# Optimization experiments

Hardware: AMD Instinct MI355X
Metric: run time of the kernel (lower is better)

## Reference

```python
import jax, jax.numpy as jnp
import numpy as np

S, B, E, H, V, L = 512, 64, 512, 768, 32000, 32
PAD_WORD, PAD_LABEL = 1, 0
PAD_BIAS = 10000.0


def _linear_init(key, fin, fout):
    # matches torch nn.Linear default U(-1/sqrt(fin), 1/sqrt(fin))
    kw, kb = jax.random.split(key)
    s = 1.0 / np.sqrt(fin)
    W = jax.random.uniform(kw, (fin, fout), minval=-s, maxval=s, dtype=jnp.float32)
    b = jax.random.uniform(kb, (fout,), minval=-s, maxval=s, dtype=jnp.float32)
    return W, b


def setup_inputs() -> dict:
    key = jax.random.key(0)
    ks = jax.random.split(key, 9)
    tokens = jax.random.randint(ks[0], (S, B), 0, V, dtype=jnp.int32)
    tags = jax.random.randint(ks[1], (S, B), 0, L, dtype=jnp.int32)
    embedding = jax.random.normal(ks[2], (V, E), dtype=jnp.float32)
    # gate order along the 4H axis: r, f, g, o (matches the 8 separate Linears, stacked)
    Wi_f, bi_f = _linear_init(ks[3], E, 4 * H)
    Wh_f, bh_f = _linear_init(ks[4], H, 4 * H)
    Wi_b, bi_b = _linear_init(ks[5], E, 4 * H)
    Wh_b, bh_b = _linear_init(ks[6], H, 4 * H)
    Wout, bout = _linear_init(ks[7], 2 * H, L)
    return {"tokens": tokens, "tags": tags, "embedding": embedding,
            "Wi_f": Wi_f, "bi_f": bi_f, "Wh_f": Wh_f, "bh_f": bh_f,
            "Wi_b": Wi_b, "bi_b": bi_b, "Wh_b": Wh_b, "bh_b": bh_b,
            "Wout": Wout, "bout": bout}


def _forward(tokens, embedding, Wi_f, bi_f, Wh_f, bh_f, Wi_b, bi_b, Wh_b, bh_b, Wout, bout):
    emb = embedding[tokens]                      # [S,B,E]
    b = tokens.shape[1]
    h = emb.shape[-1] * 0 + Wh_f.shape[0]
    # ---- forward direction: true LSTM-style recurrence ----
    xf = jnp.einsum('sbe,eg->sbg', emb, Wi_f) + bi_f   # [S,B,4H] precomputed input gates

    def step_f(carry, x):
        hid, c = carry
        g = x + hid @ Wh_f + bh_f
        r, f, gg, o = jnp.split(g, 4, axis=-1)
        c = jax.nn.sigmoid(f) * c + jax.nn.sigmoid(r) * jnp.tanh(gg)
        hid = jax.nn.sigmoid(o) * jnp.tanh(c)
        return (hid, c), hid

    z = jnp.zeros((b, h), dtype=emb.dtype)
    (hT, _), hs_f = jax.lax.scan(step_f, (z, z), xf)   # hs_f: [S,B,H]

    # ---- backward direction: source never updates `hidden`, so the hidden
    # projection uses the CONSTANT final forward hidden hT at every step.
    gb = jnp.einsum('sbe,eg->sbg', emb, Wi_b) + bi_b + hT @ Wh_b + bh_b  # [S,B,4H]
    r2, f2, g2, o2 = jnp.split(gb, 4, axis=-1)
    r2 = jax.nn.sigmoid(r2); f2 = jax.nn.sigmoid(f2)
    g2 = jnp.tanh(g2);       o2 = jax.nn.sigmoid(o2)

    def step_b(c2, gates):
        r, f, g, o = gates
        c2 = f * c2 + r * g
        return c2, o * jnp.tanh(c2)

    _, hs_b = jax.lax.scan(step_b, z, (r2, f2, g2, o2), reverse=True)  # [S,B,H], original order

    outputs = jnp.concatenate([hs_f, hs_b], axis=-1)   # [S,B,2H]
    out = outputs @ Wout + bout                        # [S,B,L]
    pad_mask = (tokens == PAD_WORD).astype(out.dtype)
    out = out.at[:, :, PAD_LABEL].add(pad_mask * PAD_BIAS)
    return out


def reference(tokens, tags, embedding, Wi_f, bi_f, Wh_f, bh_f, Wi_b, bi_b, Wh_b, bh_b, Wout, bout):
    del tags  # unused in forward, kept for signature fidelity
    return _forward(tokens, embedding, Wi_f, bi_f, Wh_f, bh_f, Wi_b, bi_b, Wh_b, bh_b, Wout, bout)
```

## Files before the change

### kernel.cpp

```cpp
#include <hip/hip_runtime.h>
#include <hip/hip_bf16.h>
#include <stdint.h>

typedef __attribute__((ext_vector_type(8))) short bf16x8;
typedef __attribute__((ext_vector_type(4))) float f32x4;
typedef __attribute__((ext_vector_type(4))) unsigned int u32x4;
typedef unsigned long long ull_t;

#define S_LEN 512
#define B_DIM 64
#define E_DIM 512
#define H_DIM 768
#define G4    3072
#define H2    1536
#define M_ROWS 32768
#define CHUNK 128
#define CM    8192
#define SLW   24
#define WPS   8
#define WPR   256
#define RWRD  4096
#define PSTR  16384
#define KRES  640
#define KREG  4
#define WROW  648
#define NTILES 1536
#define EROW  520

__device__ __forceinline__ float sigmf_(float x) { return 1.0f / (1.0f + __expf(-x)); }
__device__ __forceinline__ float tanhf2(float x) {
  x = fminf(fmaxf(x, -20.0f), 20.0f);
  float e = __expf(2.0f * x);
  return (e - 1.0f) / (e + 1.0f);
}
__device__ __forceinline__ float bfu(unsigned short u) { return __uint_as_float((unsigned)u << 16); }
__device__ __forceinline__ unsigned short packbf(float a) {
  __hip_bfloat16 t = __float2bfloat16(a);
  unsigned short b;
  __builtin_memcpy(&b, &t, 2);
  return b;
}

__global__ __launch_bounds__(256) void k_gather(const int* __restrict__ tokens,
                                                const float* __restrict__ emb,
                                                __hip_bfloat16* __restrict__ out) {
  const int t = blockIdx.x * 256 + threadIdx.x;
  const int e0 = t * 8;
  const int row = e0 >> 9;
  const int k = e0 & 511;
  const int tok = tokens[row];
  const float4* p = (const float4*)(emb + (size_t)tok * E_DIM + k);
  const float4 v0 = p[0], v1 = p[1];
  __align__(16) __hip_bfloat16 tmp[8];
  tmp[0] = __float2bfloat16(v0.x); tmp[1] = __float2bfloat16(v0.y);
  tmp[2] = __float2bfloat16(v0.z); tmp[3] = __float2bfloat16(v0.w);
  tmp[4] = __float2bfloat16(v1.x); tmp[5] = __float2bfloat16(v1.y);
  tmp[6] = __float2bfloat16(v1.z); tmp[7] = __float2bfloat16(v1.w);
  *(bf16x8*)(out + (size_t)t * 8) = *(const bf16x8*)tmp;
}

__global__ __launch_bounds__(256) void k_transpose_cast(const float* __restrict__ src,
                                                        __hip_bfloat16* __restrict__ dst,
                                                        int Rs, int Cs) {
  __shared__ float tile[32][33];
  const int tx = threadIdx.x & 31, ty = threadIdx.x >> 5;
  const int c0 = blockIdx.x * 32, r0 = blockIdx.y * 32;
  #pragma unroll
  for (int i = ty; i < 32; i += 8)
    tile[i][tx] = src[(size_t)(r0 + i) * Cs + c0 + tx];
  __syncthreads();
  #pragma unroll
  for (int i = ty; i < 32; i += 8)
    dst[(size_t)(c0 + i) * Rs + r0 + tx] = __float2bfloat16(tile[tx][i]);
}

__global__ __launch_bounds__(256) void k_bias(const float* __restrict__ bi,
                                              const float* __restrict__ bh,
                                              float* __restrict__ bias) {
  const int n = blockIdx.x * 256 + threadIdx.x;
  bias[n] = bi[n] + bh[n];
}

__device__ __forceinline__ void gemm_tile_e(char* pool, int tile,
                                            const __hip_bfloat16* __restrict__ A,
                                            const __hip_bfloat16* __restrict__ BT,
                                            const float* __restrict__ bias,
                                            __hip_bfloat16* __restrict__ C) {
  auto As = (__hip_bfloat16 (*)[40])pool;
  auto Bs = (__hip_bfloat16 (*)[40])(pool + 10240);
  const int tid = threadIdx.x;
  const int wave = tid >> 6, lane = tid & 63;
  const int q = lane >> 4, lr = lane & 15;
  const int wm = (wave >> 1) * 64, wn = (wave & 1) * 64;
  const int nb = tile % 24, mb = tile / 24;
  const int m0 = mb * 128, n0 = nb * 128;
  const int srow = tid >> 2, skseg = (tid & 3) * 8;

  f32x4 acc[4][4];
  #pragma unroll
  for (int i = 0; i < 4; ++i)
    #pragma unroll
    for (int j = 0; j < 4; ++j) { f32x4 z = {0.f, 0.f, 0.f, 0.f}; acc[i][j] = z; }

  for (int kt = 0; kt < 16; ++kt) {
    __syncthreads();
    const int kbase = kt * 32 + skseg;
    *(bf16x8*)&As[srow][skseg]      = *(const bf16x8*)(A + (size_t)(m0 + srow) * E_DIM + kbase);
    *(bf16x8*)&As[srow + 64][skseg] = *(const bf16x8*)(A + (size_t)(m0 + srow + 64) * E_DIM + kbase);
    *(bf16x8*)&Bs[srow][skseg]      = *(const bf16x8*)(BT + (size_t)(n0 + srow) * E_DIM + kbase);
    *(bf16x8*)&Bs[srow + 64][skseg] = *(const bf16x8*)(BT + (size_t)(n0 + srow + 64) * E_DIM + kbase);
    __syncthreads();
    bf16x8 af[4], bfr[4];
    #pragma unroll
    for (int mt = 0; mt < 4; ++mt) af[mt] = *(const bf16x8*)&As[wm + mt * 16 + lr][q * 8];
    #pragma unroll
    for (int nt = 0; nt < 4; ++nt) bfr[nt] = *(const bf16x8*)&Bs[wn + nt * 16 + lr][q * 8];
    #pragma unroll
    for (int mt = 0; mt < 4; ++mt)
      #pragma unroll
      for (int nt = 0; nt < 4; ++nt)
        acc[mt][nt] = __builtin_amdgcn_mfma_f32_16x16x32_bf16(af[mt], bfr[nt], acc[mt][nt], 0, 0, 0);
  }
  #pragma unroll
  for (int mt = 0; mt < 4; ++mt) {
    #pragma unroll
    for (int nt = 0; nt < 4; ++nt) {
      const int col = n0 + wn + nt * 16 + lr;
      const float bv = bias[col];
      #pragma unroll
      for (int i = 0; i < 4; ++i) {
        const int row = m0 + wm + mt * 16 + q * 4 + i;
        C[(size_t)row * G4 + col] = __float2bfloat16(acc[mt][nt][i] + bv);
      }
    }
  }
}

__device__ __forceinline__ void gemm_tile_g(char* pool, int tile,
                                            const int* __restrict__ tokens_c,
                                            const float* __restrict__ emb,
                                            const __hip_bfloat16* __restrict__ BT,
                                            const float* __restrict__ bias,
                                            __hip_bfloat16* __restrict__ C) {
  auto As = (__hip_bfloat16 (*)[40])pool;
  auto Bs = (__hip_bfloat16 (*)[40])(pool + 10240);
  const int tid = threadIdx.x;
  const int wave = tid >> 6, lane = tid & 63;
  const int q = lane >> 4, lr = lane & 15;
  const int wm = (wave >> 1) * 64, wn = (wave & 1) * 64;
  const int nb = tile % 24, mb = tile / 24;
  const int m0 = mb * 128, n0 = nb * 128;
  const int srow = tid >> 2, skseg = (tid & 3) * 8;
  const int tok0 = tokens_c[m0 + srow];
  const int tok1 = tokens_c[m0 + srow + 64];

  f32x4 acc[4][4];
  #pragma unroll
  for (int i = 0; i < 4; ++i)
    #pragma unroll
    for (int j = 0; j < 4; ++j) { f32x4 z = {0.f, 0.f, 0.f, 0.f}; acc[i][j] = z; }

  for (int kt = 0; kt < 16; ++kt) {
    __syncthreads();
    const int kbase = kt * 32 + skseg;
    {
      const float* ap = emb + (size_t)tok0 * E_DIM + kbase;
      const float4 v0 = *(const float4*)ap, v1 = *(const float4*)(ap + 4);
      __align__(16) __hip_bfloat16 t8[8];
      t8[0] = __float2bfloat16(v0.x); t8[1] = __float2bfloat16(v0.y);
      t8[2] = __float2bfloat16(v0.z); t8[3] = __float2bfloat16(v0.w);
      t8[4] = __float2bfloat16(v1.x); t8[5] = __float2bfloat16(v1.y);
      t8[6] = __float2bfloat16(v1.z); t8[7] = __float2bfloat16(v1.w);
      *(bf16x8*)&As[srow][skseg] = *(const bf16x8*)t8;
    }
    {
      const float* ap = emb + (size_t)tok1 * E_DIM + kbase;
      const float4 v0 = *(const float4*)ap, v1 = *(const float4*)(ap + 4);
      __align__(16) __hip_bfloat16 t8[8];
      t8[0] = __float2bfloat16(v0.x); t8[1] = __float2bfloat16(v0.y);
      t8[2] = __float2bfloat16(v0.z); t8[3] = __float2bfloat16(v0.w);
      t8[4] = __float2bfloat16(v1.x); t8[5] = __float2bfloat16(v1.y);
      t8[6] = __float2bfloat16(v1.z); t8[7] = __float2bfloat16(v1.w);
      *(bf16x8*)&As[srow + 64][skseg] = *(const bf16x8*)t8;
    }
    *(bf16x8*)&Bs[srow][skseg]      = *(const bf16x8*)(BT + (size_t)(n0 + srow) * E_DIM + kbase);
    *(bf16x8*)&Bs[srow + 64][skseg] = *(const bf16x8*)(BT + (size_t)(n0 + srow + 64) * E_DIM + kbase);
    __syncthreads();
    bf16x8 af[4], bfr[4];
    #pragma unroll
    for (int mt = 0; mt < 4; ++mt) af[mt] = *(const bf16x8*)&As[wm + mt * 16 + lr][q * 8];
    #pragma unroll
    for (int nt = 0; nt < 4; ++nt) bfr[nt] = *(const bf16x8*)&Bs[wn + nt * 16 + lr][q * 8];
    #pragma unroll
    for (int mt = 0; mt < 4; ++mt)
      #pragma unroll
      for (int nt = 0; nt < 4; ++nt)
        acc[mt][nt] = __builtin_amdgcn_mfma_f32_16x16x32_bf16(af[mt], bfr[nt], acc[mt][nt], 0, 0, 0);
  }
  #pragma unroll
  for (int mt = 0; mt < 4; ++mt) {
    #pragma unroll
    for (int nt = 0; nt < 4; ++nt) {
      const int col = n0 + wn + nt * 16 + lr;
      const float bv = bias[col];
      #pragma unroll
      for (int i = 0; i < 4; ++i) {
        const int row = m0 + wm + mt * 16 + q * 4 + i;
        C[(size_t)row * G4 + col] = __float2bfloat16(acc[mt][nt][i] + bv);
      }
    }
  }
}

__global__ __launch_bounds__(256) void k_gemm_e(const __hip_bfloat16* __restrict__ A,
                                                const __hip_bfloat16* __restrict__ BT,
                                                const float* __restrict__ bias,
                                                __hip_bfloat16* __restrict__ C) {
  __shared__ __align__(16) char pool[20480];
  gemm_tile_e(pool, blockIdx.x, A, BT, bias, C);
}
__global__ __launch_bounds__(256) void k_gemm_g(const int* __restrict__ tokens_c,
                                                const float* __restrict__ emb,
                                                const __hip_bfloat16* __restrict__ BT,
                                                const float* __restrict__ bias,
                                                __hip_bfloat16* __restrict__ C) {
  __shared__ __align__(16) char pool[20480];
  gemm_tile_g(pool, blockIdx.x, tokens_c, emb, BT, bias, C);
}

__device__ __forceinline__ void out_block8(char* pool, int ob,
                                           const __hip_bfloat16* __restrict__ Hs,
                                           const float* __restrict__ Wout,
                                           const float* __restrict__ bout,
                                           const int* __restrict__ tokens,
                                           float* __restrict__ out) {
  auto rowbuf = (float (*)[1536])pool;
  const int r0 = ob * 8;
  const int tid = threadIdx.x;
  for (int idx = tid; idx < 8 * 1536; idx += 256) {
    const int rr = idx / 1536, k = idx % 1536;
    rowbuf[rr][k] = __bfloat162float(Hs[(size_t)(r0 + rr) * H2 + k]);
  }
  __syncthreads();
  const int l = tid & 31, rr = tid >> 5;
  float acc = bout[l];
  #pragma unroll 8
  for (int k = 0; k < 1536; ++k) acc += rowbuf[rr][k] * Wout[k * 32 + l];
  const int row = r0 + rr;
  if (l == 0 && tokens[row] == 1) acc += 10000.0f;
  out[(size_t)row * 32 + l] = acc;
  __syncthreads();
}

__global__ __launch_bounds__(256) void k_out(const __hip_bfloat16* __restrict__ Hs,
                                             const float* __restrict__ Wout,
                                             const float* __restrict__ bout,
                                             const int* __restrict__ tokens,
                                             float* __restrict__ out) {
  __shared__ __align__(16) char pool[49152];
  out_block8(pool, blockIdx.x, Hs, Wout, bout, tokens, out);
}

__global__ __launch_bounds__(256, 1) void k_fwd_fused(const __hip_bfloat16* __restrict__ X,
                                                      const __hip_bfloat16* __restrict__ WhTf,
                                                      ull_t* __restrict__ hbuf,
                                                      __hip_bfloat16* __restrict__ Hs,
                                                      float* __restrict__ cstate,
                                                      float* __restrict__ hT,
                                                      int chunk,
                                                      const __hip_bfloat16* __restrict__ EmbA,
                                                      const int* __restrict__ tokens_nx,
                                                      const float* __restrict__ emb,
                                                      const __hip_bfloat16* __restrict__ WiT_nx,
                                                      const float* __restrict__ Bias_nx,
                                                      __hip_bfloat16* __restrict__ Xw) {
  __shared__ __align__(16) char pool[155904];
  const int bx = blockIdx.x;

  if (bx >= 128) {
    const int nw = gridDim.x - 128;
    if (EmbA) {
      for (int t = bx - 128; t < NTILES; t += nw)
        gemm_tile_e(pool, t, EmbA, WiT_nx, Bias_nx, Xw);
    } else {
      for (int t = bx - 128; t < NTILES; t += nw)
        gemm_tile_g(pool, t, tokens_nx, emb, WiT_nx, Bias_nx, Xw);
    }
    return;
  }

  unsigned short* wlds = (unsigned short*)pool;
  auto h_stage = (unsigned short (*)[776])(pool + 124416);
  auto g_lds   = (float (*)[16][26])(pool + 149248);

  const int group = bx >> 5;
  const int slice = bx & 31;
  const int r0 = group * 16;
  const int j0 = slice * SLW;
  const int tid = threadIdx.x;
  const int w = tid >> 6;
  const int lane = tid & 63;
  const int q = lane >> 4, lr = lane & 15;
  const int base = chunk * CHUNK;

  const int prow = tid >> 4;
  const int pw   = tid & 15;

  const int row  = tid >> 3;
  const int wloc = tid & 7;
  const int col0 = 3 * wloc;

  for (int c = tid; c < 96 * (KRES / 8); c += 256) {
    const int r = c / (KRES / 8), k8 = c % (KRES / 8);
    const int gate = r / SLW, n = r % SLW;
    const float4 v = *(const float4*)(WhTf + (size_t)(gate * H_DIM + j0 + n) * H_DIM + k8 * 8);
    *(float4*)(wlds + (size_t)r * WROW + k8 * 8) = v;
  }

  const int wn0 = lr;
  const int wn1 = 16 + (lr & 7);
  bf16x8 wr0[KREG], wr1[KREG];
  #pragma unroll
  for (int kk = 0; kk < KREG; ++kk) {
    const int ko = KRES + kk * 32 + q * 8;
    wr0[kk] = *(const bf16x8*)(WhTf + (size_t)(w * H_DIM + j0 + wn0) * H_DIM + ko);
    wr1[kk] = *(const bf16x8*)(WhTf + (size_t)(w * H_DIM + j0 + wn1) * H_DIM + ko);
  }

  float cr[3] = {0.f, 0.f, 0.f};
  if (tid < 128) {
    const float* cs = cstate + (size_t)(r0 + row) * H_DIM + j0 + col0;
    cr[0] = cs[0]; cr[1] = cs[1]; cr[2] = cs[2];
  }

  const unsigned skipbit = ((pw >> 2) == (slice & 3)) ? (1u << (slice >> 2)) : 0u;

  __syncthreads();

  for (int s = 0; s < CHUNK; ++s) {
    const int gs = base + s;

    unsigned short xs[4][3];
    if (tid < 128) {
      const unsigned short* xp = (const unsigned short*)(X + ((size_t)s * B_DIM + r0 + row) * G4 + j0 + col0);
      #pragma unroll
      for (int g = 0; g < 4; ++g)
        #pragma unroll
        for (int j = 0; j < 3; ++j) xs[g][j] = xp[g * H_DIM + j];
    }

    const ull_t* hc = hbuf + ((size_t)(gs & 1)) * PSTR + (size_t)group * RWRD
                    + (size_t)prow * WPR + 2 * pw;
    u32x4 d0 = {0,0,0,0}, d1 = {0,0,0,0}, d2 = {0,0,0,0}, d3 = {0,0,0,0};
    u32x4 d4 = {0,0,0,0}, d5 = {0,0,0,0}, d6 = {0,0,0,0}, d7 = {0,0,0,0};
    const unsigned pollmask = (s == 0) ? 0xFFu : (0xFFu ^ skipbit);
    {
      const unsigned e16 = (unsigned)(unsigned short)gs;
      unsigned need = pollmask;
      long guard = 0;
      for (;;) {
#define POLL_LD(i, dv) \
        if (need & (1u << (i))) \
          asm volatile("global_load_dwordx4 %0, %1, off sc0 sc1" \
                       : "=v"(dv) : "v"(hc + 32 * (i)) : "memory");
        POLL_LD(0, d0) POLL_LD(1, d1) POLL_LD(2, d2) POLL_LD(3, d3)
        POLL_LD(4, d4) POLL_LD(5, d5) POLL_LD(6, d6) POLL_LD(7, d7)
#undef POLL_LD
        asm volatile("s_waitcnt vmcnt(0)"
                     : "+v"(d0), "+v"(d1), "+v"(d2), "+v"(d3),
                       "+v"(d4), "+v"(d5), "+v"(d6), "+v"(d7)
                     :: "memory");
        unsigned nn = 0;
#define POLL_CK(i, dv) \
        if ((need & (1u << (i))) && \
            ((((dv).x & 0xFFFFu) != e16) || (((dv).z & 0xFFFFu) != e16))) nn |= 1u << (i);
        POLL_CK(0, d0) POLL_CK(1, d1) POLL_CK(2, d2) POLL_CK(3, d3)
        POLL_CK(4, d4) POLL_CK(5, d5) POLL_CK(6, d6) POLL_CK(7, d7)
#undef POLL_CK
        need = nn;
        if (!need) break;
        if (++guard > (1L << 20)) break;
        __builtin_amdgcn_s_sleep(1);
      }
    }
    {
#define STAGE_PAIR(i, dv) \
      if (pollmask & (1u << (i))) { \
        unsigned* hp = (unsigned*)&h_stage[prow][6 * pw + 96 * (i)]; \
        hp[0] = ((dv).x >> 16) | ((dv).y << 16); \
        hp[1] = ((dv).y >> 16) | ((dv).z & 0xFFFF0000u); \
        hp[2] = (dv).w; \
      }
      STAGE_PAIR(0, d0) STAGE_PAIR(1, d1) STAGE_PAIR(2, d2) STAGE_PAIR(3, d3)
      STAGE_PAIR(4, d4) STAGE_PAIR(5, d5) STAGE_PAIR(6, d6) STAGE_PAIR(7, d7)
#undef STAGE_PAIR
    }
    __syncthreads();

    f32x4 acc0 = {0.f, 0.f, 0.f, 0.f};
    f32x4 acc1 = {0.f, 0.f, 0.f, 0.f};
    {
      const unsigned short* wb = wlds + (size_t)w * SLW * WROW;
      #pragma unroll
      for (int kt = 0; kt < KRES / 32; ++kt) {
        const int ko = kt * 32 + q * 8;
        const bf16x8 a  = *(const bf16x8*)&h_stage[lr][ko];
        const bf16x8 b0 = *(const bf16x8*)(wb + (size_t)wn0 * WROW + ko);
        const bf16x8 b1 = *(const bf16x8*)(wb + (size_t)wn1 * WROW + ko);
        acc0 = __builtin_amdgcn_mfma_f32_16x16x32_bf16(a, b0, acc0, 0, 0, 0);
        acc1 = __builtin_amdgcn_mfma_f32_16x16x32_bf16(a, b1, acc1, 0, 0, 0);
      }
      #pragma unroll
      for (int kk = 0; kk < KREG; ++kk) {
        const bf16x8 a = *(const bf16x8*)&h_stage[lr][KRES + kk * 32 + q * 8];
        acc0 = __builtin_amdgcn_mfma_f32_16x16x32_bf16(a, wr0[kk], acc0, 0, 0, 0);
        acc1 = __builtin_amdgcn_mfma_f32_16x16x32_bf16(a, wr1[kk], acc1, 0, 0, 0);
      }
    }
    #pragma unroll
    for (int i = 0; i < 4; ++i) g_lds[w][q * 4 + i][lr] = acc0[i];
    if (lr < 8) {
      #pragma unroll
      for (int i = 0; i < 4; ++i) g_lds[w][q * 4 + i][16 + lr] = acc1[i];
    }
    __syncthreads();

    if (tid < 128) {
      float h[3];
      #pragma unroll
      for (int j = 0; j < 3; ++j) {
        const float rv = g_lds[0][row][col0 + j] + bfu(xs[0][j]);
        const float fv = g_lds[1][row][col0 + j] + bfu(xs[1][j]);
        const float gv = g_lds[2][row][col0 + j] + bfu(xs[2][j]);
        const float ov = g_lds[3][row][col0 + j] + bfu(xs[3][j]);
        const float c = sigmf_(fv) * cr[j] + sigmf_(rv) * tanhf2(gv);
        cr[j] = c;
        h[j] = sigmf_(ov) * tanhf2(c);
      }
      const unsigned short b0 = packbf(h[0]), b1 = packbf(h[1]), b2 = packbf(h[2]);
      const ull_t wv = (ull_t)(unsigned short)(gs + 1)
                     | ((ull_t)b0 << 16) | ((ull_t)b1 << 32) | ((ull_t)b2 << 48);
      __hip_atomic_store(hbuf + ((size_t)((gs + 1) & 1)) * PSTR + (size_t)group * RWRD
                         + (size_t)row * WPR + slice * WPS + wloc,
                         wv, __ATOMIC_RELAXED, __HIP_MEMORY_SCOPE_AGENT);
      h_stage[row][j0 + col0]     = b0;
      h_stage[row][j0 + col0 + 1] = b1;
      h_stage[row][j0 + col0 + 2] = b2;
      unsigned short* hsp = (unsigned short*)(Hs + ((size_t)gs * B_DIM + r0 + row) * H2 + j0 + col0);
      hsp[0] = b0; hsp[1] = b1; hsp[2] = b2;
      if (chunk == 3 && s == CHUNK - 1) {
        float* hp = hT + (size_t)(r0 + row) * H_DIM + j0 + col0;
        hp[0] = h[0]; hp[1] = h[1]; hp[2] = h[2];
      }
    }
  }

  if (tid < 128) {
    float* cs = cstate + (size_t)(r0 + row) * H_DIM + j0 + col0;
    cs[0] = cr[0]; cs[1] = cr[1]; cs[2] = cr[2];
  }
}

__global__ __launch_bounds__(256) void k_hTW(const float* __restrict__ hT,
                                             const float* __restrict__ Whb,
                                             float* __restrict__ hTW) {
  const int b = blockIdx.y;
  const int n = blockIdx.x * 256 + threadIdx.x;
  __shared__ float hs[768];
  for (int i = threadIdx.x; i < 768; i += 256) hs[i] = hT[b * 768 + i];
  __syncthreads();
  float acc = 0.f;
  #pragma unroll 4
  for (int k = 0; k < 768; ++k) acc += hs[k] * Whb[(size_t)k * G4 + n];
  hTW[(size_t)b * G4 + n] = acc;
}

__global__ __launch_bounds__(256, 1) void k_bwd_fused3(const __hip_bfloat16* __restrict__ Emb,
                                                       const __hip_bfloat16* __restrict__ WiTb,
                                                       const float* __restrict__ BiasB,
                                                       const float* __restrict__ hTW,
                                                       __hip_bfloat16* __restrict__ Hs,
                                                       float* __restrict__ c2state,
                                                       int chunk) {
  __shared__ __align__(16) unsigned short wlds[96 * EROW];
  __shared__ __align__(16) unsigned short emb_s[2][16][EROW];
  __shared__ float g_lds[4][16][26];

  const int bx = blockIdx.x;
  const int group = bx >> 5;
  const int slice = bx & 31;
  const int r0 = group * 8;
  const int j0 = slice * SLW;
  const int tid = threadIdx.x;
  const int w = tid >> 6;
  const int lane = tid & 63;
  const int q = lane >> 4, lr = lane & 15;
  const int base = chunk * CHUNK;

  for (int c = tid; c < 96 * 64; c += 256) {
    const int r = c >> 6, k8 = c & 63;
    const int gate = r / SLW, n = r % SLW;
    *(float4*)(wlds + (size_t)r * EROW + k8 * 8) =
        *(const float4*)(WiTb + (size_t)(gate * H_DIM + j0 + n) * E_DIM + k8 * 8);
  }

  const int rr = tid >> 3, wloc = tid & 7, col0 = 3 * wloc;
  float hw0[3], hw1[3], hw2[3], hw3[3], c2r[3] = {0.f, 0.f, 0.f};
  if (tid < 64) {
    const int b = r0 + rr;
    #pragma unroll
    for (int j = 0; j < 3; ++j) {
      const int n = j0 + col0 + j;
      hw0[j] = BiasB[n]        + hTW[(size_t)b * G4 + n];
      hw1[j] = BiasB[768 + n]  + hTW[(size_t)b * G4 + 768 + n];
      hw2[j] = BiasB[1536 + n] + hTW[(size_t)b * G4 + 1536 + n];
      hw3[j] = BiasB[2304 + n] + hTW[(size_t)b * G4 + 2304 + n];
      c2r[j] = c2state[(size_t)b * H_DIM + n];
    }
  }
  const int wn0 = lr;
  const int wn1 = 16 + (lr & 7);
  const unsigned short* wb0 = wlds + (size_t)(w * SLW + wn0) * EROW;
  const unsigned short* wb1 = wlds + (size_t)(w * SLW + wn1) * EROW;

  int aa[4], kk8[4];
  #pragma unroll
  for (int i = 0; i < 4; ++i) { aa[i] = (tid + 256 * i) >> 6; kk8[i] = (tid + 256 * i) & 63; }

  bf16x8 pf0, pf1, pf2, pf3;
#define PF_LOAD(t) { \
    pf0 = *(const bf16x8*)(Emb + ((size_t)(base + 2*(t)+1-(aa[0]>>3)) * B_DIM + r0 + (aa[0]&7)) * E_DIM + kk8[0]*8); \
    pf1 = *(const bf16x8*)(Emb + ((size_t)(base + 2*(t)+1-(aa[1]>>3)) * B_DIM + r0 + (aa[1]&7)) * E_DIM + kk8[1]*8); \
    pf2 = *(const bf16x8*)(Emb + ((size_t)(base + 2*(t)+1-(aa[2]>>3)) * B_DIM + r0 + (aa[2]&7)) * E_DIM + kk8[2]*8); \
    pf3 = *(const bf16x8*)(Emb + ((size_t)(base + 2*(t)+1-(aa[3]>>3)) * B_DIM + r0 + (aa[3]&7)) * E_DIM + kk8[3]*8); }

  PF_LOAD(CHUNK / 2 - 1);

  int buf = 0;
  for (int t = CHUNK / 2 - 1; t >= 0; --t) {
    *(bf16x8*)&emb_s[buf][aa[0]][kk8[0] * 8] = pf0;
    *(bf16x8*)&emb_s[buf][aa[1]][kk8[1] * 8] = pf1;
    *(bf16x8*)&emb_s[buf][aa[2]][kk8[2] * 8] = pf2;
    *(bf16x8*)&emb_s[buf][aa[3]][kk8[3] * 8] = pf3;
    if (t > 0) PF_LOAD(t - 1);
    __syncthreads();

    f32x4 a0 = {0.f, 0.f, 0.f, 0.f};
    f32x4 a1 = {0.f, 0.f, 0.f, 0.f};
    #pragma unroll
    for (int kt = 0; kt < 16; ++kt) {
      const int ko = kt * 32 + q * 8;
      const bf16x8 av = *(const bf16x8*)&emb_s[buf][lr][ko];
      const bf16x8 b0 = *(const bf16x8*)(wb0 + ko);
      const bf16x8 b1 = *(const bf16x8*)(wb1 + ko);
      a0 = __builtin_amdgcn_mfma_f32_16x16x32_bf16(av, b0, a0, 0, 0, 0);
      a1 = __builtin_amdgcn_mfma_f32_16x16x32_bf16(av, b1, a1, 0, 0, 0);
    }
    #pragma unroll
    for (int i = 0; i < 4; ++i) g_lds[w][q * 4 + i][lr] = a0[i];
    if (lr < 8) {
      #pragma unroll
      for (int i = 0; i < 4; ++i) g_lds[w][q * 4 + i][16 + lr] = a1[i];
    }
    __syncthreads();

    if (tid < 64) {
      #pragma unroll
      for (int st = 0; st < 2; ++st) {
        const int gs = base + 2 * t + 1 - st;
        const int m = st * 8 + rr;
        unsigned short hb[3];
        #pragma unroll
        for (int j = 0; j < 3; ++j) {
          const float rv = sigmf_(g_lds[0][m][col0 + j] + hw0[j]);
          const float fv = sigmf_(g_lds[1][m][col0 + j] + hw1[j]);
          const float gv = tanhf2(g_lds[2][m][col0 + j] + hw2[j]);
          const float ov = sigmf_(g_lds[3][m][col0 + j] + hw3[j]);
          c2r[j] = fv * c2r[j] + rv * gv;
          hb[j] = packbf(ov * tanhf2(c2r[j]));
        }
        unsigned short* hsp = (unsigned short*)(Hs + ((size_t)gs * B_DIM + r0 + rr) * H2
                                                + H_DIM + j0 + col0);
        hsp[0] = hb[0]; hsp[1] = hb[1]; hsp[2] = hb[2];
      }
    }
    buf ^= 1;
  }
#undef PF_LOAD

  if (tid < 64) {
    #pragma unroll
    for (int j = 0; j < 3; ++j)
      c2state[(size_t)(r0 + rr) * H_DIM + j0 + col0 + j] = c2r[j];
  }
}

__global__ __launch_bounds__(256) void k_bwd_scan(const __hip_bfloat16* __restrict__ X,
                                                  const float* __restrict__ hTW,
                                                  __hip_bfloat16* __restrict__ Hs,
                                                  float* __restrict__ c2state,
                                                  int chunk) {
  const int t = blockIdx.x * 256 + threadIdx.x;
  const int b = t / H_DIM;
  const int j = t % H_DIM;
  const int base = chunk * CHUNK;
  const float hw0 = hTW[(size_t)b * G4 + j];
  const float hw1 = hTW[(size_t)b * G4 + 768 + j];
  const float hw2 = hTW[(size_t)b * G4 + 1536 + j];
  const float hw3 = hTW[(size_t)b * G4 + 2304 + j];
  float c2 = c2state[t];
  for (int s = CHUNK - 1; s >= 0; --s) {
    const size_t xb = ((size_t)s * B_DIM + b) * G4 + j;
    const float r = sigmf_(__bfloat162float(X[xb]) + hw0);
    const float f = sigmf_(__bfloat162float(X[xb + 768]) + hw1);
    const float g = tanhf2(__bfloat162float(X[xb + 1536]) + hw2);
    const float o = sigmf_(__bfloat162float(X[xb + 2304]) + hw3);
    c2 = f * c2 + r * g;
    Hs[((size_t)(base + s) * B_DIM + b) * H2 + H_DIM + j] = __float2bfloat16(o * tanhf2(c2));
  }
  c2state[t] = c2;
}

extern "C" void kernel_launch(void* const* d_in, const int* in_sizes, int n_in,
                              void* d_out, int out_size, void* d_ws, size_t ws_size,
                              hipStream_t stream) {
  const int*   tokens = (const int*)d_in[0];
  const float* emb    = (const float*)d_in[2];
  const float* Wi_f   = (const float*)d_in[3];
  const float* bi_f   = (const float*)d_in[4];
  const float* Wh_f   = (const float*)d_in[5];
  const float* bh_f   = (const float*)d_in[6];
  const float* Wi_b   = (const float*)d_in[7];
  const float* bi_b   = (const float*)d_in[8];
  const float* Wh_b   = (const float*)d_in[9];
  const float* bh_b   = (const float*)d_in[10];
  const float* Wout   = (const float*)d_in[11];
  const float* bout   = (const float*)d_in[12];
  float* out = (float*)d_out;
  char* ws = (char*)d_ws;

  size_t off = 0;
  auto alloc = [&](size_t bytes) { size_t o = off; off += (bytes + 255) & ~(size_t)255; return o; };
  const size_t oHs    = alloc((size_t)M_ROWS * H2 * 2);
  const size_t oX0    = alloc((size_t)CM * G4 * 2);
  const size_t oWhTf  = alloc((size_t)G4 * H_DIM * 2);
  const size_t oWiTf  = alloc((size_t)G4 * E_DIM * 2);
  const size_t oWiTb  = alloc((size_t)G4 * E_DIM * 2);
  const size_t oBiasF = alloc((size_t)G4 * 4);
  const size_t oBiasB = alloc((size_t)G4 * 4);
  const size_t oHbuf  = alloc((size_t)2 * PSTR * 8);
  const size_t oCst   = alloc((size_t)B_DIM * H_DIM * 4);
  const size_t oHT    = alloc((size_t)B_DIM * H_DIM * 4);
  const size_t oHTW   = alloc((size_t)B_DIM * G4 * 4);
  const size_t oC2    = alloc((size_t)B_DIM * H_DIM * 4);
  const size_t oX1    = alloc((size_t)CM * G4 * 2);
  const bool overlap = (off <= ws_size);
  const size_t oEmb   = alloc((size_t)M_ROWS * E_DIM * 2);
  const bool tierA = (off <= ws_size);
  (void)in_sizes; (void)n_in; (void)out_size;

  __hip_bfloat16* Hs   = (__hip_bfloat16*)(ws + oHs);
  __hip_bfloat16* X0   = (__hip_bfloat16*)(ws + oX0);
  __hip_bfloat16* X1   = overlap ? (__hip_bfloat16*)(ws + oX1) : X0;
  __hip_bfloat16* Emb  = tierA ? (__hip_bfloat16*)(ws + oEmb) : (__hip_bfloat16*)nullptr;
  __hip_bfloat16* WhTf = (__hip_bfloat16*)(ws + oWhTf);
  __hip_bfloat16* WiTf = (__hip_bfloat16*)(ws + oWiTf);
  __hip_bfloat16* WiTb = (__hip_bfloat16*)(ws + oWiTb);
  float*          BiasF= (float*)(ws + oBiasF);
  float*          BiasB= (float*)(ws + oBiasB);
  ull_t*          Hbuf = (ull_t*)(ws + oHbuf);
  float*          Cst  = (float*)(ws + oCst);
  float*          HT   = (float*)(ws + oHT);
  float*          HTW  = (float*)(ws + oHTW);
  float*          C2   = (float*)(ws + oC2);

  hipMemsetAsync(ws + oHbuf, 0, (size_t)2 * PSTR * 8, stream);
  hipMemsetAsync(ws + oCst, 0, (size_t)B_DIM * H_DIM * 4, stream);
  hipMemsetAsync(ws + oC2, 0, (size_t)B_DIM * H_DIM * 4, stream);

  if (tierA)
    k_gather<<<8192, 256, 0, stream>>>(tokens, emb, Emb);
  k_transpose_cast<<<dim3(96, 24), 256, 0, stream>>>(Wh_f, WhTf, 768, 3072);
  k_transpose_cast<<<dim3(96, 16), 256, 0, stream>>>(Wi_f, WiTf, 512, 3072);
  k_transpose_cast<<<dim3(96, 16), 256, 0, stream>>>(Wi_b, WiTb, 512, 3072);
  k_bias<<<12, 256, 0, stream>>>(bi_f, bh_f, BiasF);
  k_bias<<<12, 256, 0, stream>>>(bi_b, bh_b, BiasB);

  if (overlap && tierA) {
    k_gemm_e<<<NTILES, 256, 0, stream>>>(Emb, WiTf, BiasF, X0);
    auto EA = [&](int c) { return Emb + (size_t)c * CM * E_DIM; };
    k_fwd_fused<<<240, 256, 0, stream>>>(X0, WhTf, Hbuf, Hs, Cst, HT, 0,
                                         EA(1), tokens, emb, WiTf, BiasF, X1);
    k_fwd_fused<<<240, 256, 0, stream>>>(X1, WhTf, Hbuf, Hs, Cst, HT, 1,
                                         EA(2), tokens, emb, WiTf, BiasF, X0);
    k_fwd_fused<<<240, 256, 0, stream>>>(X0, WhTf, Hbuf, Hs, Cst, HT, 2,
                                         EA(3), tokens, emb, WiTf, BiasF, X1);
    k_fwd_fused<<<128, 256, 0, stream>>>(X1, WhTf, Hbuf, Hs, Cst, HT, 3,
                                         EA(0), tokens, emb, WiTf, BiasF, X0);
    k_hTW<<<dim3(12, 64), 256, 0, stream>>>(HT, Wh_b, HTW);
    k_bwd_fused3<<<256, 256, 0, stream>>>(Emb, WiTb, BiasB, HTW, Hs, C2, 3);
    k_bwd_fused3<<<256, 256, 0, stream>>>(Emb, WiTb, BiasB, HTW, Hs, C2, 2);
    k_bwd_fused3<<<256, 256, 0, stream>>>(Emb, WiTb, BiasB, HTW, Hs, C2, 1);
    k_bwd_fused3<<<256, 256, 0, stream>>>(Emb, WiTb, BiasB, HTW, Hs, C2, 0);
    k_out<<<4096, 256, 0, stream>>>(Hs, Wout, bout, tokens, out);
  } else if (overlap) {
    k_gemm_g<<<NTILES, 256, 0, stream>>>(tokens, emb, WiTf, BiasF, X0);
    k_fwd_fused<<<240, 256, 0, stream>>>(X0, WhTf, Hbuf, Hs, Cst, HT, 0,
                                         nullptr, tokens + 1 * CM, emb, WiTf, BiasF, X1);
    k_fwd_fused<<<240, 256, 0, stream>>>(X1, WhTf, Hbuf, Hs, Cst, HT, 1,
                                         nullptr, tokens + 2 * CM, emb, WiTf, BiasF, X0);
    k_fwd_fused<<<240, 256, 0, stream>>>(X0, WhTf, Hbuf, Hs, Cst, HT, 2,
                                         nullptr, tokens + 3 * CM, emb, WiTf, BiasF, X1);
    k_fwd_fused<<<240, 256, 0, stream>>>(X1, WhTf, Hbuf, Hs, Cst, HT, 3,
                                         nullptr, tokens + 3 * CM, emb, WiTb, BiasB, X0);
    k_hTW<<<dim3(12, 64), 256, 0, stream>>>(HT, Wh_b, HTW);
    k_bwd_scan<<<192, 256, 0, stream>>>(X0, HTW, Hs, C2, 3);
    for (int c = 2; c >= 0; --c) {
      k_gemm_g<<<NTILES, 256, 0, stream>>>(tokens + (size_t)c * CM, emb, WiTb, BiasB, X1);
      k_bwd_scan<<<192, 256, 0, stream>>>(X1, HTW, Hs, C2, c);
    }
    k_out<<<4096, 256, 0, stream>>>(Hs, Wout, bout, tokens, out);
  } else {
    for (int c = 0; c < 4; ++c) {
      k_gemm_g<<<NTILES, 256, 0, stream>>>(tokens + (size_t)c * CM, emb, WiTf, BiasF, X0);
      k_fwd_fused<<<128, 256, 0, stream>>>(X0, WhTf, Hbuf, Hs, Cst, HT, c,
                                           nullptr, tokens, emb, WiTf, BiasF, X0);
    }
    k_hTW<<<dim3(12, 64), 256, 0, stream>>>(HT, Wh_b, HTW);
    for (int c = 3; c >= 0; --c) {
      k_gemm_g<<<NTILES, 256, 0, stream>>>(tokens + (size_t)c * CM, emb, WiTb, BiasB, X0);
      k_bwd_scan<<<192, 256, 0, stream>>>(X0, HTW, Hs, C2, c);
    }
    k_out<<<4096, 256, 0, stream>>>(Hs, Wout, bout, tokens, out);
  }
}
```

Baseline: 3.135 ms.

## Overlap backward input GEMMs and output projection with forward recurrence blocks

When workspace allows two extra gate buffers, the idle GEMM blocks of the forward recurrent kernels also precompute backward-direction input gates for chunks 3 and 2. The first two backward chunks then run as lightweight scans, with extra blocks computing the output projection for the already-finished chunk 3. The final k_out covers only the remaining chunks. The aim is to hide backward GEMM and output-projection work behind the latency-bound forward scan, at the cost of more workspace and more work in the side blocks. It also moves the barrier in bwd_fused3 ahead of the next prefetch.

```diff
diff --git a/kernel.cpp b/kernel.cpp
--- a/kernel.cpp
+++ b/kernel.cpp
@@ -273,7 +273,11 @@
                                                       const float* __restrict__ emb,
                                                       const __hip_bfloat16* __restrict__ WiT_nx,
                                                       const float* __restrict__ Bias_nx,
-                                                      __hip_bfloat16* __restrict__ Xw) {
+                                                      __hip_bfloat16* __restrict__ Xw,
+                                                      const __hip_bfloat16* __restrict__ EmbB,
+                                                      const __hip_bfloat16* __restrict__ WiTb2,
+                                                      const float* __restrict__ BiasB2,
+                                                      __hip_bfloat16* __restrict__ Xb) {
   __shared__ __align__(16) char pool[155904];
   const int bx = blockIdx.x;
 
@@ -285,6 +289,10 @@
     } else {
       for (int t = bx - 128; t < NTILES; t += nw)
         gemm_tile_g(pool, t, tokens_nx, emb, WiT_nx, Bias_nx, Xw);
+    }
+    if (EmbB && Xb) {
+      for (int t = bx - 128; t < NTILES; t += nw)
+        gemm_tile_e(pool, t, EmbB, WiTb2, BiasB2, Xb);
     }
     return;
   }
@@ -542,8 +550,9 @@
     *(bf16x8*)&emb_s[buf][aa[1]][kk8[1] * 8] = pf1;
     *(bf16x8*)&emb_s[buf][aa[2]][kk8[2] * 8] = pf2;
     *(bf16x8*)&emb_s[buf][aa[3]][kk8[3] * 8] = pf3;
+    __syncthreads();
+
     if (t > 0) PF_LOAD(t - 1);
-    __syncthreads();
 
     f32x4 a0 = {0.f, 0.f, 0.f, 0.f};
     f32x4 a1 = {0.f, 0.f, 0.f, 0.f};
@@ -595,12 +604,24 @@
   }
 }
 
-__global__ __launch_bounds__(256) void k_bwd_scan(const __hip_bfloat16* __restrict__ X,
-                                                  const float* __restrict__ hTW,
-                                                  __hip_bfloat16* __restrict__ Hs,
-                                                  float* __restrict__ c2state,
-                                                  int chunk) {
-  const int t = blockIdx.x * 256 + threadIdx.x;
+__global__ __launch_bounds__(256) void k_bwd_scan_o(const __hip_bfloat16* __restrict__ X,
+                                                    const float* __restrict__ hTW,
+                                                    __hip_bfloat16* __restrict__ Hs,
+                                                    float* __restrict__ c2state,
+                                                    int chunk, int out_chunk,
+                                                    const float* __restrict__ Wout,
+                                                    const float* __restrict__ bout,
+                                                    const int* __restrict__ tokens,
+                                                    float* __restrict__ out) {
+  __shared__ __align__(16) char pool[49152];
+  const int bx = blockIdx.x;
+  if (bx >= 192) {
+    if (out_chunk >= 0)
+      for (int ob = bx - 192; ob < 1024; ob += 128)
+        out_block8(pool, out_chunk * 1024 + ob, Hs, Wout, bout, tokens, out);
+    return;
+  }
+  const int t = bx * 256 + threadIdx.x;
   const int b = t / H_DIM;
   const int j = t % H_DIM;
   const int base = chunk * CHUNK;
@@ -657,12 +678,17 @@
   const bool overlap = (off <= ws_size);
   const size_t oEmb   = alloc((size_t)M_ROWS * E_DIM * 2);
   const bool tierA = (off <= ws_size);
+  const size_t oX2    = alloc((size_t)CM * G4 * 2);
+  const size_t oX3    = alloc((size_t)CM * G4 * 2);
+  const bool tierX = (off <= ws_size);
   (void)in_sizes; (void)n_in; (void)out_size;
 
   __hip_bfloat16* Hs   = (__hip_bfloat16*)(ws + oHs);
   __hip_bfloat16* X0   = (__hip_bfloat16*)(ws + oX0);
   __hip_bfloat16* X1   = overlap ? (__hip_bfloat16*)(ws + oX1) : X0;
   __hip_bfloat16* Emb  = tierA ? (__hip_bfloat16*)(ws + oEmb) : (__hip_bfloat16*)nullptr;
+  __hip_bfloat16* X2   = tierX ? (__hip_bfloat16*)(ws + oX2) : (__hip_bfloat16*)nullptr;
+  __hip_bfloat16* X3   = tierX ? (__hip_bfloat16*)(ws + oX3) : (__hip_bfloat16*)nullptr;
   __hip_bfloat16* WhTf = (__hip_bfloat16*)(ws + oWhTf);
   __hip_bfloat16* WiTf = (__hip_bfloat16*)(ws + oWiTf);
   __hip_bfloat16* WiTb = (__hip_bfloat16*)(ws + oWiTb);
@@ -686,17 +712,42 @@
   k_bias<<<12, 256, 0, stream>>>(bi_f, bh_f, BiasF);
   k_bias<<<12, 256, 0, stream>>>(bi_b, bh_b, BiasB);
 
-  if (overlap && tierA) {
+  auto EA = [&](int c) { return Emb + (size_t)c * CM * E_DIM; };
+
+  if (tierX) {
     k_gemm_e<<<NTILES, 256, 0, stream>>>(Emb, WiTf, BiasF, X0);
-    auto EA = [&](int c) { return Emb + (size_t)c * CM * E_DIM; };
     k_fwd_fused<<<240, 256, 0, stream>>>(X0, WhTf, Hbuf, Hs, Cst, HT, 0,
-                                         EA(1), tokens, emb, WiTf, BiasF, X1);
+                                         EA(1), tokens, emb, WiTf, BiasF, X1,
+                                         EA(3), WiTb, BiasB, X2);
     k_fwd_fused<<<240, 256, 0, stream>>>(X1, WhTf, Hbuf, Hs, Cst, HT, 1,
-                                         EA(2), tokens, emb, WiTf, BiasF, X0);
+                                         EA(2), tokens, emb, WiTf, BiasF, X3,
+                                         EA(2), WiTb, BiasB, X0);
+    k_fwd_fused<<<240, 256, 0, stream>>>(X3, WhTf, Hbuf, Hs, Cst, HT, 2,
+                                         EA(3), tokens, emb, WiTf, BiasF, X1,
+                                         nullptr, nullptr, nullptr, nullptr);
+    k_fwd_fused<<<128, 256, 0, stream>>>(X1, WhTf, Hbuf, Hs, Cst, HT, 3,
+                                         EA(0), tokens, emb, WiTf, BiasF, X0,
+                                         nullptr, nullptr, nullptr, nullptr);
+    k_hTW<<<dim3(12, 64), 256, 0, stream>>>(HT, Wh_b, HTW);
+    k_bwd_scan_o<<<320, 256, 0, stream>>>(X2, HTW, Hs, C2, 3, -1, Wout, bout, tokens, out);
+    k_bwd_scan_o<<<320, 256, 0, stream>>>(X0, HTW, Hs, C2, 2, 3, Wout, bout, tokens, out);
+    k_bwd_fused3<<<256, 256, 0, stream>>>(Emb, WiTb, BiasB, HTW, Hs, C2, 1);
+    k_bwd_fused3<<<256, 256, 0, stream>>>(Emb, WiTb, BiasB, HTW, Hs, C2, 0);
+    k_out<<<3072, 256, 0, stream>>>(Hs, Wout, bout, tokens, out);
+  } else if (tierA) {
+    k_gemm_e<<<NTILES, 256, 0, stream>>>(Emb, WiTf, BiasF, X0);
+    k_fwd_fused<<<240, 256, 0, stream>>>(X0, WhTf, Hbuf, Hs, Cst, HT, 0,
+                                         EA(1), tokens, emb, WiTf, BiasF, X1,
+                                         nullptr, nullptr, nullptr, nullptr);
+    k_fwd_fused<<<240, 256, 0, stream>>>(X1, WhTf, Hbuf, Hs, Cst, HT, 1,
+                                         EA(2), tokens, emb, WiTf, BiasF, X0,
+                                         nullptr, nullptr, nullptr, nullptr);
     k_fwd_fused<<<240, 256, 0, stream>>>(X0, WhTf, Hbuf, Hs, Cst, HT, 2,
-                                         EA(3), tokens, emb, WiTf, BiasF, X1);
+                                         EA(3), tokens, emb, WiTf, BiasF, X1,
+                                         nullptr, nullptr, nullptr, nullptr);
     k_fwd_fused<<<128, 256, 0, stream>>>(X1, WhTf, Hbuf, Hs, Cst, HT, 3,
-                                         EA(0), tokens, emb, WiTf, BiasF, X0);
+                                         EA(0), tokens, emb, WiTf, BiasF, X0,
+                                         nullptr, nullptr, nullptr, nullptr);
     k_hTW<<<dim3(12, 64), 256, 0, stream>>>(HT, Wh_b, HTW);
     k_bwd_fused3<<<256, 256, 0, stream>>>(Emb, WiTb, BiasB, HTW, Hs, C2, 3);
     k_bwd_fused3<<<256, 256, 0, stream>>>(Emb, WiTb, BiasB, HTW, Hs, C2, 2);
@@ -706,30 +757,35 @@
   } else if (overlap) {
     k_gemm_g<<<NTILES, 256, 0, stream>>>(tokens, emb, WiTf, BiasF, X0);
     k_fwd_fused<<<240, 256, 0, stream>>>(X0, WhTf, Hbuf, Hs, Cst, HT, 0,
-                                         nullptr, tokens + 1 * CM, emb, WiTf, BiasF, X1);
+                                         nullptr, tokens + 1 * CM, emb, WiTf, BiasF, X1,
+                                         nullptr, nullptr, nullptr, nullptr);
     k_fwd_fused<<<240, 256, 0, stream>>>(X1, WhTf, Hbuf, Hs, Cst, HT, 1,
-                                         nullptr, tokens + 2 * CM, emb, WiTf, BiasF, X0);
+                                         nullptr, tokens + 2 * CM, emb, WiTf, BiasF, X0,
+                                         nullptr, nullptr, nullptr, nullptr);
     k_fwd_fused<<<240, 256, 0, stream>>>(X0, WhTf, Hbuf, Hs, Cst, HT, 2,
-                                         nullptr, tokens + 3 * CM, emb, WiTf, BiasF, X1);
+                                         nullptr, tokens + 3 * CM, emb, WiTf, BiasF, X1,
+                                         nullptr, nullptr, nullptr, nullptr);
     k_fwd_fused<<<240, 256, 0, stream>>>(X1, WhTf, Hbuf, Hs, Cst, HT, 3,
-                                         nullptr, tokens + 3 * CM, emb, WiTb, BiasB, X0);
+                                         nullptr, tokens + 3 * CM, emb, WiTb, BiasB, X0,
+                                         nullptr, nullptr, nullptr, nullptr);
     k_hTW<<<dim3(12, 64), 256, 0, stream>>>(HT, Wh_b, HTW);
-    k_bwd_scan<<<192, 256, 0, stream>>>(X0, HTW, Hs, C2, 3);
+    k_bwd_scan_o<<<192, 256, 0, stream>>>(X0, HTW, Hs, C2, 3, -1, Wout, bout, tokens, out);
     for (int c = 2; c >= 0; --c) {
       k_gemm_g<<<NTILES, 256, 0, stream>>>(tokens + (size_t)c * CM, emb, WiTb, BiasB, X1);
-      k_bwd_scan<<<192, 256, 0, stream>>>(X1, HTW, Hs, C2, c);
+      k_bwd_scan_o<<<192, 256, 0, stream>>>(X1, HTW, Hs, C2, c, -1, Wout, bout, tokens, out);
     }
     k_out<<<4096, 256, 0, stream>>>(Hs, Wout, bout, tokens, out);
   } else {
     for (int c = 0; c < 4; ++c) {
       k_gemm_g<<<NTILES, 256, 0, stream>>>(tokens + (size_t)c * CM, emb, WiTf, BiasF, X0);
       k_fwd_fused<<<128, 256, 0, stream>>>(X0, WhTf, Hbuf, Hs, Cst, HT, c,
-                                           nullptr, tokens, emb, WiTf, BiasF, X0);
+                                           nullptr, tokens, emb, WiTf, BiasF, X0,
+                                           nullptr, nullptr, nullptr, nullptr);
     }
     k_hTW<<<dim3(12, 64), 256, 0, stream>>>(HT, Wh_b, HTW);
     for (int c = 3; c >= 0; --c) {
       k_gemm_g<<<NTILES, 256, 0, stream>>>(tokens + (size_t)c * CM, emb, WiTb, BiasB, X0);
-      k_bwd_scan<<<192, 256, 0, stream>>>(X0, HTW, Hs, C2, c);
+      k_bwd_scan_o<<<192, 256, 0, stream>>>(X0, HTW, Hs, C2, c, -1, Wout, bout, tokens, out);
     }
     k_out<<<4096, 256, 0, stream>>>(Hs, Wout, bout, tokens, out);
   }
```

New measurement: 3.145 ms. No clear change (+0.3%).
